# Performance work log

Measured on AMD Instinct MI355X. Metric: run time of the kernel, lower is better.

The kernel has to match this reference:

```python
import jax, jax.numpy as jnp
import numpy as np


def setup_inputs() -> dict:
    key = jax.random.key(0)
    k1, k2 = jax.random.split(key)
    x = jax.random.normal(k1, (8, 3, 4096), dtype=jnp.float32)
    y = jax.random.normal(k2, (8, 3, 4096), dtype=jnp.float32)
    return {"x": x, "y": y}


def reference(x, y):
    # x: [B, dim, N], y: [B, dim, M]
    num_points_x = x.shape[2]
    num_points_y = y.shape[2]
    xx = jnp.sum(x * x, axis=1)              # [B, N]
    yy = jnp.sum(y * y, axis=1)              # [B, M]
    zz = jnp.einsum('bdn,bdm->bnm', x, y)    # [B, N, M]
    P = xx[:, :, None] + yy[:, None, :] - 2.0 * zz  # squared pairwise distances
    min_for_each_x = jnp.min(P, axis=2)      # [B, N]
    min_for_each_y = jnp.min(P, axis=1)      # [B, M]
    Ls1s2 = jnp.sum(min_for_each_x, axis=1) / num_points_x
    Ls2s1 = jnp.sum(min_for_each_y, axis=1) / num_points_y
    # variant 'cd-t'
    distance = Ls1s2 + Ls2s1
    return jnp.mean(distance)
```

## Files before the change

### kernel.cpp

```cpp
#include <hip/hip_runtime.h>

#define NB 8
#define NPTS 4096
#define IPT 4
#define OUT_SCALE (1.0f / (float)(NPTS * NB))

template <int CH_>
__global__ __launch_bounds__(256) void chamfer_main(
    const float* __restrict__ x, const float* __restrict__ y,
    float* __restrict__ pmin, float* __restrict__ out) {
    constexpr int MCHUNK = NPTS / CH_;
    __shared__ float4 qs[MCHUNK];

    const int b   = blockIdx.y;
    const int z   = blockIdx.z;
    const int dir = z / CH_;
    const int ch  = z % CH_;
    const int tid = threadIdx.x;

    const float* A = (dir == 0) ? x : y;
    const float* B = (dir == 0) ? y : x;

    if (blockIdx.x == 0 && b == 0 && z == 0 && tid == 0) out[0] = 0.0f;

    const float* bb = B + (size_t)b * 3 * NPTS + (size_t)ch * MCHUNK;
    for (int t = tid; t < MCHUNK; t += 256) {
        float bxv = bb[t];
        float byv = bb[NPTS + t];
        float bzv = bb[2 * NPTS + t];
        qs[t] = make_float4(-2.0f * bxv, -2.0f * byv, -2.0f * bzv,
                            bxv * bxv + byv * byv + bzv * bzv);
    }

    const int i0 = blockIdx.x * (256 * IPT) + tid;
    const float* ab = A + (size_t)b * 3 * NPTS;
    float ax[IPT], ay[IPT], az[IPT], xx[IPT], vmin[IPT];
#pragma unroll
    for (int k = 0; k < IPT; ++k) {
        int i = i0 + k * 256;
        ax[k] = ab[i];
        ay[k] = ab[NPTS + i];
        az[k] = ab[2 * NPTS + i];
        xx[k] = ax[k] * ax[k] + ay[k] * ay[k] + az[k] * az[k];
        vmin[k] = 3.4e38f;
    }
    __syncthreads();

    for (int m = 0; m < MCHUNK; m += 4) {
        float t[4][IPT];
#pragma unroll
        for (int u = 0; u < 4; ++u) {
            float4 c = qs[m + u];
#pragma unroll
            for (int k = 0; k < IPT; ++k) {
                float s = xx[k] + c.w;
                s = fmaf(ax[k], c.x, s);
                s = fmaf(ay[k], c.y, s);
                t[u][k] = fmaf(az[k], c.z, s);
            }
        }
#pragma unroll
        for (int k = 0; k < IPT; ++k) {
            float m01 = fminf(t[0][k], t[1][k]);
            float m23 = fminf(t[2][k], t[3][k]);
            vmin[k] = fminf(vmin[k], fminf(m01, m23));
        }
    }

    float* pout = pmin + ((size_t)(dir * NB + b) * CH_ + ch) * NPTS;
#pragma unroll
    for (int k = 0; k < IPT; ++k) pout[i0 + k * 256] = vmin[k];
}

template <int CH_>
__global__ __launch_bounds__(256) void chamfer_reduce(
    const float* __restrict__ pmin, float* __restrict__ out) {
    __shared__ float sred[4];
    const int u  = blockIdx.x * 256 + threadIdx.x;
    const int i  = u & (NPTS - 1);
    const int db = u >> 12;
    const float* base = pmin + (size_t)db * CH_ * NPTS + i;
    float vm = base[0];
#pragma unroll
    for (int c = 1; c < CH_; ++c) vm = fminf(vm, base[(size_t)c * NPTS]);

    float s = vm;
#pragma unroll
    for (int off = 32; off > 0; off >>= 1) s += __shfl_down(s, off, 64);
    const int lane = threadIdx.x & 63;
    const int wid  = threadIdx.x >> 6;
    if (lane == 0) sred[wid] = s;
    __syncthreads();
    if (threadIdx.x == 0) {
        float tot = sred[0] + sred[1] + sred[2] + sred[3];
        atomicAdd(out, tot * OUT_SCALE);
    }
}

__global__ void zero_out(float* out) { out[0] = 0.0f; }

__global__ __launch_bounds__(256) void chamfer_direct(
    const float* __restrict__ x, const float* __restrict__ y,
    float* __restrict__ out) {
    const int b   = blockIdx.y;
    const int dir = blockIdx.z;
    const float* A  = (dir == 0) ? x : y;
    const float* Bm = (dir == 0) ? y : x;
    const int i = blockIdx.x * blockDim.x + threadIdx.x;
    const float* abase = A + (size_t)b * 3 * NPTS + i;
    const float ax = abase[0], ay = abase[NPTS], az = abase[2 * NPTS];
    const float* bbase = Bm + (size_t)b * 3 * NPTS;
    float vmin = 3.4e38f;
#pragma unroll 8
    for (int m = 0; m < NPTS; ++m) {
        float dx = ax - bbase[m];
        float dy = ay - bbase[NPTS + m];
        float dz = az - bbase[2 * NPTS + m];
        float t = dx * dx;
        t = fmaf(dy, dy, t);
        t = fmaf(dz, dz, t);
        vmin = fminf(vmin, t);
    }
    float s = vmin;
#pragma unroll
    for (int off = 32; off > 0; off >>= 1) s += __shfl_down(s, off, 64);
    if ((threadIdx.x & 63) == 0) atomicAdd(out, s * OUT_SCALE);
}

extern "C" void kernel_launch(void* const* d_in, const int* in_sizes, int n_in,
                              void* d_out, int out_size, void* d_ws, size_t ws_size,
                              hipStream_t stream) {
    const float* x = (const float*)d_in[0];
    const float* y = (const float*)d_in[1];
    float* out  = (float*)d_out;
    float* pmin = (float*)d_ws;

    const dim3 blk(256);
    const int gx = NPTS / (256 * IPT);

    const size_t need32 = 2ull * NB * 32 * NPTS * sizeof(float);
    const size_t need8  = 2ull * NB * 8  * NPTS * sizeof(float);

    if (ws_size >= need32) {
        chamfer_main<32><<<dim3(gx, NB, 2 * 32), blk, 0, stream>>>(x, y, pmin, out);
        chamfer_reduce<32><<<dim3((2 * NB * NPTS) / 256), blk, 0, stream>>>(pmin, out);
    } else if (ws_size >= need8) {
        chamfer_main<8><<<dim3(gx, NB, 2 * 8), blk, 0, stream>>>(x, y, pmin, out);
        chamfer_reduce<8><<<dim3((2 * NB * NPTS) / 256), blk, 0, stream>>>(pmin, out);
    } else {
        zero_out<<<dim3(1), dim3(1), 0, stream>>>(out);
        chamfer_direct<<<dim3(NPTS / 256, NB, 2), blk, 0, stream>>>(x, y, out);
    }
}
```

Baseline: 87.69 us.

## Vectorize chamfer inner loop with packed float2 FMA and hoist norm add

Rewrites the inner distance loop to use two-wide float vectors so the compiler can emit packed FP32 FMA and min instructions (v_pk_fma_f32). Each thread now handles 8 points instead of 4. The per-point norm xx is pulled out of the min and added once at the end, which removes one add per pair. Shared memory now stores the query coefficients duplicated into pairs, doubling LDS footprint and read traffic. Grid x shrinks to 2 blocks per batch/chunk, and register pressure goes up.

```diff
diff --git a/kernel.cpp b/kernel.cpp
--- a/kernel.cpp
+++ b/kernel.cpp
@@ -2,15 +2,33 @@
 
 #define NB 8
 #define NPTS 4096
-#define IPT 4
+#define IPT 8
+#define NPAIR (IPT / 2)
 #define OUT_SCALE (1.0f / (float)(NPTS * NB))
+
+typedef float v2f __attribute__((ext_vector_type(2)));
+
+#if defined(__has_builtin) && __has_builtin(__builtin_elementwise_fma)
+#define V2FMA(a, b, c) __builtin_elementwise_fma((a), (b), (c))
+#else
+static __device__ inline v2f V2FMA(v2f a, v2f b, v2f c) {
+    v2f r; r.x = fmaf(a.x, b.x, c.x); r.y = fmaf(a.y, b.y, c.y); return r;
+}
+#endif
+#if defined(__has_builtin) && __has_builtin(__builtin_elementwise_min)
+#define V2MIN(a, b) __builtin_elementwise_min((a), (b))
+#else
+static __device__ inline v2f V2MIN(v2f a, v2f b) {
+    v2f r; r.x = fminf(a.x, b.x); r.y = fminf(a.y, b.y); return r;
+}
+#endif
 
 template <int CH_>
 __global__ __launch_bounds__(256) void chamfer_main(
     const float* __restrict__ x, const float* __restrict__ y,
     float* __restrict__ pmin, float* __restrict__ out) {
     constexpr int MCHUNK = NPTS / CH_;
-    __shared__ float4 qs[MCHUNK];
+    __shared__ v2f qs[MCHUNK * 4];
 
     const int b   = blockIdx.y;
     const int z   = blockIdx.z;
@@ -28,48 +46,50 @@
         float bxv = bb[t];
         float byv = bb[NPTS + t];
         float bzv = bb[2 * NPTS + t];
-        qs[t] = make_float4(-2.0f * bxv, -2.0f * byv, -2.0f * bzv,
-                            bxv * bxv + byv * byv + bzv * bzv);
+        float w = bxv * bxv + byv * byv + bzv * bzv;
+        qs[4 * t + 0] = v2f{-2.0f * bxv, -2.0f * bxv};
+        qs[4 * t + 1] = v2f{-2.0f * byv, -2.0f * byv};
+        qs[4 * t + 2] = v2f{-2.0f * bzv, -2.0f * bzv};
+        qs[4 * t + 3] = v2f{w, w};
     }
 
     const int i0 = blockIdx.x * (256 * IPT) + tid;
     const float* ab = A + (size_t)b * 3 * NPTS;
-    float ax[IPT], ay[IPT], az[IPT], xx[IPT], vmin[IPT];
+    v2f ax2[NPAIR], ay2[NPAIR], az2[NPAIR], xx2[NPAIR], vmin2[NPAIR];
 #pragma unroll
-    for (int k = 0; k < IPT; ++k) {
-        int i = i0 + k * 256;
-        ax[k] = ab[i];
-        ay[k] = ab[NPTS + i];
-        az[k] = ab[2 * NPTS + i];
-        xx[k] = ax[k] * ax[k] + ay[k] * ay[k] + az[k] * az[k];
-        vmin[k] = 3.4e38f;
+    for (int p = 0; p < NPAIR; ++p) {
+        int ia = i0 + (2 * p) * 256;
+        int ib = i0 + (2 * p + 1) * 256;
+        ax2[p] = v2f{ab[ia],            ab[ib]};
+        ay2[p] = v2f{ab[NPTS + ia],     ab[NPTS + ib]};
+        az2[p] = v2f{ab[2 * NPTS + ia], ab[2 * NPTS + ib]};
+        xx2[p] = V2FMA(ax2[p], ax2[p], V2FMA(ay2[p], ay2[p], az2[p] * az2[p]));
+        vmin2[p] = v2f{3.4e38f, 3.4e38f};
     }
     __syncthreads();
 
-    for (int m = 0; m < MCHUNK; m += 4) {
-        float t[4][IPT];
+    for (int m = 0; m < MCHUNK; m += 2) {
+        v2f cx0 = qs[4 * m + 0], cy0 = qs[4 * m + 1], cz0 = qs[4 * m + 2], cw0 = qs[4 * m + 3];
+        v2f cx1 = qs[4 * m + 4], cy1 = qs[4 * m + 5], cz1 = qs[4 * m + 6], cw1 = qs[4 * m + 7];
 #pragma unroll
-        for (int u = 0; u < 4; ++u) {
-            float4 c = qs[m + u];
-#pragma unroll
-            for (int k = 0; k < IPT; ++k) {
-                float s = xx[k] + c.w;
-                s = fmaf(ax[k], c.x, s);
-                s = fmaf(ay[k], c.y, s);
-                t[u][k] = fmaf(az[k], c.z, s);
-            }
-        }
-#pragma unroll
-        for (int k = 0; k < IPT; ++k) {
-            float m01 = fminf(t[0][k], t[1][k]);
-            float m23 = fminf(t[2][k], t[3][k]);
-            vmin[k] = fminf(vmin[k], fminf(m01, m23));
+        for (int p = 0; p < NPAIR; ++p) {
+            v2f t0 = V2FMA(ax2[p], cx0, cw0);
+            t0 = V2FMA(ay2[p], cy0, t0);
+            t0 = V2FMA(az2[p], cz0, t0);
+            v2f t1 = V2FMA(ax2[p], cx1, cw1);
+            t1 = V2FMA(ay2[p], cy1, t1);
+            t1 = V2FMA(az2[p], cz1, t1);
+            vmin2[p] = V2MIN(vmin2[p], V2MIN(t0, t1));
         }
     }
 
     float* pout = pmin + ((size_t)(dir * NB + b) * CH_ + ch) * NPTS;
 #pragma unroll
-    for (int k = 0; k < IPT; ++k) pout[i0 + k * 256] = vmin[k];
+    for (int p = 0; p < NPAIR; ++p) {
+        v2f r = vmin2[p] + xx2[p];
+        pout[i0 + (2 * p) * 256]     = r.x;
+        pout[i0 + (2 * p + 1) * 256] = r.y;
+    }
 }
 
 template <int CH_>
```

Result: faster. 83.50 us (-4.8%).
